# Kernel optimization log

Measured on AMD Instinct MI355X. Metric: run time of the kernel, lower is better.

Reference implementation:

```python
import jax, jax.numpy as jnp
import numpy as np

N, IN_F, HID, HEADS, OUT = 50000, 128, 32, 4, 40
E = 800000
LN_EPS = 1e-5


def setup_inputs() -> dict:
    key = jax.random.key(0)
    ks = jax.random.split(key, 16)
    d1 = HEADS * HID  # 128
    s_in = 1.0 / np.sqrt(IN_F)
    s_d1 = 1.0 / np.sqrt(d1)
    return {
        "x": jax.random.normal(ks[0], (N, IN_F), jnp.float32),
        "edge_index": jax.random.randint(ks[1], (2, E), 0, N, jnp.int64),
        # layer 1 (GATv2, heads=4, concat=True)
        "Wl1": jax.random.normal(ks[2], (IN_F, d1), jnp.float32) * s_in,
        "bl1": jnp.zeros((d1,), jnp.float32),
        "Wr1": jax.random.normal(ks[3], (IN_F, d1), jnp.float32) * s_in,
        "br1": jnp.zeros((d1,), jnp.float32),
        "att1": jax.random.normal(ks[4], (HEADS, HID), jnp.float32) * s_d1,
        "b1": jnp.zeros((d1,), jnp.float32),
        # LayerNorm over hidden_channels*heads
        "g1": jnp.ones((d1,), jnp.float32),
        "be1": jnp.zeros((d1,), jnp.float32),
        # layer 2 (GATv2, heads=1, concat=False)
        "Wl2": jax.random.normal(ks[5], (d1, OUT), jnp.float32) * s_d1,
        "bl2": jnp.zeros((OUT,), jnp.float32),
        "Wr2": jax.random.normal(ks[6], (d1, OUT), jnp.float32) * s_d1,
        "br2": jnp.zeros((OUT,), jnp.float32),
        "att2": jax.random.normal(ks[7], (1, OUT), jnp.float32) / np.sqrt(OUT),
        "b2": jnp.zeros((OUT,), jnp.float32),
    }


def gatv2(x, src, tgt, Wl, bl, Wr, br, att, bias, heads, C, concat):
    n = x.shape[0]
    xl = (x @ Wl + bl).reshape(n, heads, C)  # source transform
    xr = (x @ Wr + br).reshape(n, heads, C)  # target transform
    h = xl[src] + xr[tgt]                    # [E,H,C]
    e = jnp.sum(jax.nn.leaky_relu(h, 0.2) * att, axis=-1)  # [E,H]
    # segment softmax over edges sharing the same target node
    m = jax.ops.segment_max(e, tgt, num_segments=n)        # [N,H]
    m = jnp.where(jnp.isfinite(m), m, 0.0)
    p = jnp.exp(e - m[tgt])
    s = jax.ops.segment_sum(p, tgt, num_segments=n)
    alpha = p / (s[tgt] + 1e-16)                           # [E,H]
    out = jax.ops.segment_sum(alpha[..., None] * xl[src], tgt, num_segments=n)  # [N,H,C]
    out = out.reshape(n, heads * C) if concat else out.mean(axis=1)
    return out + bias


def layer_norm(x, g, b):
    mu = x.mean(-1, keepdims=True)
    var = x.var(-1, keepdims=True)
    return (x - mu) * jax.lax.rsqrt(var + LN_EPS) * g + b


def reference(x, edge_index, Wl1, bl1, Wr1, br1, att1, b1, g1, be1,
              Wl2, bl2, Wr2, br2, att2, b2):
    src, tgt = edge_index[0], edge_index[1]
    h = gatv2(x, src, tgt, Wl1, bl1, Wr1, br1, att1, b1, HEADS, HID, True)
    h = jax.nn.elu(layer_norm(h, g1, be1))
    # dropout is identity in eval mode
    return gatv2(h, src, tgt, Wl2, bl2, Wr2, br2, att2, b2, 1, OUT, False)
```

## Files before the change

kernel.cpp:

```cpp
#include <hip/hip_runtime.h>
#include <hip/hip_bf16.h>
#include <math.h>

#define NN 50000
#define EE 800000
#define NB_SCAN 49

typedef __attribute__((ext_vector_type(8))) short bf16x8;
typedef __attribute__((ext_vector_type(4))) float f32x4;
typedef __attribute__((ext_vector_type(2))) float f32x2;
typedef __attribute__((ext_vector_type(8))) unsigned short ushortx8;

#define OFF_XBF  ((size_t)0)
#define SZ_XBF   ((size_t)NN * 128 * 2)
#define OFF_XL1B (OFF_XBF + SZ_XBF)
#define SZ_XL1B  ((size_t)NN * 128 * 2)
#define OFF_XR1  (OFF_XL1B + SZ_XL1B)
#define SZ_XR1   ((size_t)NN * 128 * 4)
#define OFF_H1B  (OFF_XR1 + SZ_XR1)
#define SZ_H1B   ((size_t)NN * 128 * 2)
#define OFF_XL2B (OFF_H1B + SZ_H1B)
#define SZ_XL2B  ((size_t)NN * 40 * 2)
#define OFF_XR2  (OFF_XL2B + SZ_XL2B)
#define SZ_XR2   ((size_t)NN * 40 * 4)
#define OFF_BP1  (OFF_XR2 + SZ_XR2)
#define SZ_BP1   ((size_t)32768 * 2)
#define OFF_BP2  (OFF_BP1 + SZ_BP1)
#define SZ_BP2   ((size_t)10240 * 2)
#define OFF_BB1  (OFF_BP2 + SZ_BP2)
#define SZ_BB1   ((size_t)1024)
#define OFF_BB2  (OFF_BB1 + SZ_BB1)
#define SZ_BB2   ((size_t)512)
#define OFF_DEG  (OFF_BB2 + SZ_BB2)
#define SZ_DEG   ((size_t)NN * 4)
#define OFF_OFFS (OFF_DEG + SZ_DEG)
#define SZ_OFFS  ((size_t)200192)
#define OFF_CUR  (OFF_OFFS + SZ_OFFS)
#define SZ_CUR   ((size_t)NN * 4)
#define OFF_CSR  (OFF_CUR + SZ_CUR)
#define SZ_CSR   ((size_t)EE * 4)
#define OFF_BSUM (OFF_CSR + SZ_CSR)
#define SZ_BSUM  ((size_t)256)

__device__ __forceinline__ unsigned short f2bf(float f) {
    union { float f; unsigned u; } v;
    v.f = f;
    unsigned r = v.u + 0x7fffu + ((v.u >> 16) & 1u);
    return (unsigned short)(r >> 16);
}
__device__ __forceinline__ f32x2 bf2f2(unsigned u) {
    union { unsigned u; float f; } lo, hi;
    lo.u = u << 16;
    hi.u = u & 0xffff0000u;
    f32x2 r;
    r.x = lo.f;
    r.y = hi.f;
    return r;
}

__device__ __forceinline__ f32x2 pk_add(f32x2 a, f32x2 b) {
    f32x2 d;
    asm("v_pk_add_f32 %0, %1, %2" : "=v"(d) : "v"(a), "v"(b));
    return d;
}
__device__ __forceinline__ f32x2 pk_mul(f32x2 a, f32x2 b) {
    f32x2 d;
    asm("v_pk_mul_f32 %0, %1, %2" : "=v"(d) : "v"(a), "v"(b));
    return d;
}
__device__ __forceinline__ f32x2 pk_fma(f32x2 a, f32x2 b, f32x2 c) {
    f32x2 d;
    asm("v_pk_fma_f32 %0, %1, %2, %3" : "=v"(d) : "v"(a), "v"(b), "v"(c));
    return d;
}
__device__ __forceinline__ f32x2 pk_abs2(f32x2 a) {
    f32x2 r;
    r.x = __builtin_fabsf(a.x);
    r.y = __builtin_fabsf(a.y);
    return r;
}

__global__ void prep_kernel(
    const float* __restrict__ x, unsigned short* __restrict__ XBF,
    const float* __restrict__ Wl1, const float* __restrict__ bl1,
    const float* __restrict__ Wr1, const float* __restrict__ br1,
    const float* __restrict__ Wl2, const float* __restrict__ bl2,
    const float* __restrict__ Wr2, const float* __restrict__ br2,
    unsigned short* __restrict__ BP1, float* __restrict__ BB1,
    unsigned short* __restrict__ BP2, float* __restrict__ BB2,
    int* __restrict__ DEG) {
    int i = blockIdx.x * blockDim.x + threadIdx.x;
    if (i < NN * 128 / 8) {
        const float4* p = (const float4*)x + (size_t)i * 2;
        float4 v0 = p[0], v1 = p[1];
        ushortx8 o;
        o[0] = f2bf(v0.x); o[1] = f2bf(v0.y); o[2] = f2bf(v0.z); o[3] = f2bf(v0.w);
        o[4] = f2bf(v1.x); o[5] = f2bf(v1.y); o[6] = f2bf(v1.z); o[7] = f2bf(v1.w);
        *((ushortx8*)XBF + i) = o;
    }
    if (i < NN) DEG[i] = 0;
    if (i < 32768) {
        int j = i & 7, l = (i >> 3) & 63, nt = (i >> 9) & 15, kt = i >> 13;
        int k = kt * 32 + ((l >> 4) << 3) + j;
        int n = nt * 16 + (l & 15);
        float v = (n < 128) ? Wl1[k * 128 + n] : Wr1[k * 128 + (n - 128)];
        BP1[i] = f2bf(v);
    }
    if (i < 10240) {
        int j = i & 7, l = (i >> 3) & 63;
        int rest = i >> 9;
        int nt = rest % 5, kt = rest / 5;
        int k = kt * 32 + ((l >> 4) << 3) + j;
        int n = nt * 16 + (l & 15);
        float v = (n < 40) ? Wl2[k * 40 + n] : Wr2[k * 40 + (n - 40)];
        BP2[i] = f2bf(v);
    }
    if (i < 256) BB1[i] = (i < 128) ? bl1[i] : br1[i - 128];
    if (i < 80) BB2[i] = (i < 40) ? bl2[i] : br2[i - 40];
}

__global__ void hist_kernel(const int* __restrict__ tgts, int* __restrict__ deg, int e_) {
    int e = blockIdx.x * blockDim.x + threadIdx.x;
    if (e < e_) atomicAdd(&deg[tgts[e]], 1);
}

__global__ __launch_bounds__(1024) void scan_bsum_kernel(
    const int* __restrict__ deg, int* __restrict__ bsum, int n) {
    __shared__ int ws[16];
    int lane = threadIdx.x & 63, w = threadIdx.x >> 6;
    int i = blockIdx.x * 1024 + threadIdx.x;
    int v = (i < n) ? deg[i] : 0;
#pragma unroll
    for (int d = 32; d >= 1; d >>= 1) v += __shfl_xor(v, d, 64);
    if (lane == 0) ws[w] = v;
    __syncthreads();
    if (threadIdx.x < 16) {
        int xv = ws[threadIdx.x];
#pragma unroll
        for (int d = 8; d >= 1; d >>= 1) xv += __shfl_xor(xv, d, 16);
        if (threadIdx.x == 0) bsum[blockIdx.x] = xv;
    }
}

__global__ void scan_boff_kernel(int* __restrict__ bsum, int nb) {
    int tid = threadIdx.x;
    int v = (tid < nb) ? bsum[tid] : 0;
    int incl = v;
#pragma unroll
    for (int d = 1; d < 64; d <<= 1) {
        int t = __shfl_up(incl, d, 64);
        if (tid >= d) incl += t;
    }
    if (tid < nb) bsum[tid] = incl - v;
}

__global__ __launch_bounds__(1024) void scan_final_kernel(
    const int* __restrict__ deg, const int* __restrict__ bsum,
    int* __restrict__ off, int* __restrict__ cur, int n) {
    __shared__ int wsum[16];
    int lane = threadIdx.x & 63, w = threadIdx.x >> 6;
    int carry = bsum[blockIdx.x];
    int i = blockIdx.x * 1024 + threadIdx.x;
    int v = (i < n) ? deg[i] : 0;
    int incl = v;
#pragma unroll
    for (int d = 1; d < 64; d <<= 1) {
        int t = __shfl_up(incl, d, 64);
        if (lane >= d) incl += t;
    }
    if (lane == 63) wsum[w] = incl;
    __syncthreads();
    if (threadIdx.x < 16) {
        int xv = wsum[threadIdx.x];
#pragma unroll
        for (int d = 1; d < 16; d <<= 1) {
            int t = __shfl_up(xv, d, 16);
            if ((int)threadIdx.x >= d) xv += t;
        }
        wsum[threadIdx.x] = xv;
    }
    __syncthreads();
    int add = (w > 0) ? wsum[w - 1] : 0;
    if (i < n) {
        int tot = carry + incl + add;
        off[i + 1] = tot;
        cur[i] = tot - v;
    }
    if (i == 0) off[0] = 0;
}

__global__ void scatter_kernel(const int* __restrict__ srcs, const int* __restrict__ tgts,
                               int* __restrict__ cur, int* __restrict__ csr, int e_) {
    int e = blockIdx.x * blockDim.x + threadIdx.x;
    if (e < e_) {
        int t = tgts[e];
        int pos = atomicAdd(&cur[t], 1);
        csr[pos] = srcs[e];
    }
}

__global__ __launch_bounds__(256) void gemm_mfma_kernel(
    const unsigned short* __restrict__ Abf, const unsigned short* __restrict__ BP,
    const float* __restrict__ bias, unsigned short* __restrict__ Cbf,
    float* __restrict__ Cf, int M, int NT, int NSPLIT) {
    int wave = (blockIdx.x * blockDim.x + threadIdx.x) >> 6;
    int lane = threadIdx.x & 63;
    int r0 = wave * 16;
    if (r0 >= M) return;
    int koff = (lane >> 4) << 3;
    const unsigned short* ap = &Abf[(size_t)(r0 + (lane & 15)) * 128 + koff];
    bf16x8 a0 = *(const bf16x8*)(ap);
    bf16x8 a1 = *(const bf16x8*)(ap + 32);
    bf16x8 a2 = *(const bf16x8*)(ap + 64);
    bf16x8 a3 = *(const bf16x8*)(ap + 96);
    int NR = (NT << 4) - NSPLIT;
    int col = lane & 15;
    int rb = r0 + ((lane >> 4) << 2);
    size_t ktStride = (size_t)NT * 512;
    for (int nt = 0; nt < NT; ++nt) {
        const unsigned short* bp = &BP[((size_t)nt * 64 + lane) * 8];
        f32x4 acc = {0.f, 0.f, 0.f, 0.f};
        acc = __builtin_amdgcn_mfma_f32_16x16x32_bf16(a0, *(const bf16x8*)(bp), acc, 0, 0, 0);
        acc = __builtin_amdgcn_mfma_f32_16x16x32_bf16(a1, *(const bf16x8*)(bp + ktStride), acc, 0, 0, 0);
        acc = __builtin_amdgcn_mfma_f32_16x16x32_bf16(a2, *(const bf16x8*)(bp + 2 * ktStride), acc, 0, 0, 0);
        acc = __builtin_amdgcn_mfma_f32_16x16x32_bf16(a3, *(const bf16x8*)(bp + 3 * ktStride), acc, 0, 0, 0);
        int c = (nt << 4) + col;
        float bb = bias[c];
        if (c < NSPLIT) {
#pragma unroll
            for (int j = 0; j < 4; ++j) Cbf[(size_t)(rb + j) * NSPLIT + c] = f2bf(acc[j] + bb);
        } else {
#pragma unroll
            for (int j = 0; j < 4; ++j) Cf[(size_t)(rb + j) * NR + (c - NSPLIT)] = acc[j] + bb;
        }
    }
}

__global__ __launch_bounds__(256) void gat_edge1_kernel(
    const unsigned short* __restrict__ XL1B, const float* __restrict__ XR1,
    const int* __restrict__ off, const int* __restrict__ csr,
    const float* __restrict__ att, const float* __restrict__ b1,
    const float* __restrict__ g1, const float* __restrict__ be1,
    unsigned short* __restrict__ H1B) {
    int wid = threadIdx.x >> 6;
    int lane = threadIdx.x & 63;
    int node = blockIdx.x * 4 + wid;
    if (node >= NN) return;
    int grp = lane >> 4;
    int sub = lane & 15;
    int cbase = sub << 3;
    const float* xrrow = &XR1[(size_t)node * 128];
    float4 xrA = *(const float4*)&xrrow[cbase];
    float4 xrB = *(const float4*)&xrrow[cbase + 4];
    float4 atA = *(const float4*)&att[cbase];
    float4 atB = *(const float4*)&att[cbase + 4];
    f32x2 xr01 = {xrA.x, xrA.y}, xr23 = {xrA.z, xrA.w};
    f32x2 xr45 = {xrB.x, xrB.y}, xr67 = {xrB.z, xrB.w};
    f32x2 a06_01 = {0.6f * atA.x, 0.6f * atA.y}, a06_23 = {0.6f * atA.z, 0.6f * atA.w};
    f32x2 a06_45 = {0.6f * atB.x, 0.6f * atB.y}, a06_67 = {0.6f * atB.z, 0.6f * atB.w};
    f32x2 a04_01 = {0.4f * atA.x, 0.4f * atA.y}, a04_23 = {0.4f * atA.z, 0.4f * atA.w};
    f32x2 a04_45 = {0.4f * atB.x, 0.4f * atB.y}, a04_67 = {0.4f * atB.z, 0.4f * atB.w};
    f32x2 acc01 = {0.f, 0.f}, acc23 = {0.f, 0.f}, acc45 = {0.f, 0.f}, acc67 = {0.f, 0.f};
    float s = 0.f;
    int jb = off[node], je = off[node + 1];
    int nb = (je - jb + 3) >> 2;
#pragma unroll 2
    for (int k = 0; k < nb; ++k) {
        int eidx = jb + (k << 2) + grp;
        int src = csr[min(eidx, je - 1)];
        uint4 q = *(const uint4*)&XL1B[(size_t)src * 128 + cbase];
        f32x2 xl01 = bf2f2(q.x), xl23 = bf2f2(q.y), xl45 = bf2f2(q.z), xl67 = bf2f2(q.w);
        f32x2 h01 = pk_add(xl01, xr01);
        f32x2 h23 = pk_add(xl23, xr23);
        f32x2 h45 = pk_add(xl45, xr45);
        f32x2 h67 = pk_add(xl67, xr67);
        f32x2 t2 = pk_mul(h01, a06_01);
        t2 = pk_fma(pk_abs2(h01), a04_01, t2);
        t2 = pk_fma(h23, a06_23, t2);
        t2 = pk_fma(pk_abs2(h23), a04_23, t2);
        t2 = pk_fma(h45, a06_45, t2);
        t2 = pk_fma(pk_abs2(h45), a04_45, t2);
        t2 = pk_fma(h67, a06_67, t2);
        t2 = pk_fma(pk_abs2(h67), a04_67, t2);
        float t = t2.x + t2.y;
        t += __shfl_xor(t, 1, 64);
        t += __shfl_xor(t, 2, 64);
        t = (eidx < je) ? t : -1e30f;
        float p = __expf(t);
        f32x2 pp;
        pp.x = p;
        pp.y = p;
        acc01 = pk_fma(pp, xl01, acc01);
        acc23 = pk_fma(pp, xl23, acc23);
        acc45 = pk_fma(pp, xl45, acc45);
        acc67 = pk_fma(pp, xl67, acc67);
        s += p;
    }
    float a0 = acc01.x, a1 = acc01.y, a2 = acc23.x, a3 = acc23.y;
    float a4 = acc45.x, a5 = acc45.y, a6 = acc67.x, a7 = acc67.y;
#pragma unroll
    for (int d = 16; d <= 32; d <<= 1) {
        s += __shfl_xor(s, d, 64);
        a0 += __shfl_xor(a0, d, 64);
        a1 += __shfl_xor(a1, d, 64);
        a2 += __shfl_xor(a2, d, 64);
        a3 += __shfl_xor(a3, d, 64);
        a4 += __shfl_xor(a4, d, 64);
        a5 += __shfl_xor(a5, d, 64);
        a6 += __shfl_xor(a6, d, 64);
        a7 += __shfl_xor(a7, d, 64);
    }
    float inv = 1.f / (s + 1e-16f);
    float4 bA = *(const float4*)&b1[cbase];
    float4 bB = *(const float4*)&b1[cbase + 4];
    float o[8];
    o[0] = a0 * inv + bA.x;
    o[1] = a1 * inv + bA.y;
    o[2] = a2 * inv + bA.z;
    o[3] = a3 * inv + bA.w;
    o[4] = a4 * inv + bB.x;
    o[5] = a5 * inv + bB.y;
    o[6] = a6 * inv + bB.z;
    o[7] = a7 * inv + bB.w;
    float sum = 0.f, sq = 0.f;
#pragma unroll
    for (int j = 0; j < 8; ++j) {
        sum += o[j];
        sq = fmaf(o[j], o[j], sq);
    }
#pragma unroll
    for (int d = 1; d <= 8; d <<= 1) {
        sum += __shfl_xor(sum, d, 64);
        sq += __shfl_xor(sq, d, 64);
    }
    float mu = sum * (1.f / 128.f);
    float var = sq * (1.f / 128.f) - mu * mu;
    float rs = rsqrtf(var + 1e-5f);
    if (grp == 0) {
        float4 gA = *(const float4*)&g1[cbase];
        float4 gB = *(const float4*)&g1[cbase + 4];
        float4 eA = *(const float4*)&be1[cbase];
        float4 eB = *(const float4*)&be1[cbase + 4];
        float y[8];
        y[0] = (o[0] - mu) * rs * gA.x + eA.x;
        y[1] = (o[1] - mu) * rs * gA.y + eA.y;
        y[2] = (o[2] - mu) * rs * gA.z + eA.z;
        y[3] = (o[3] - mu) * rs * gA.w + eA.w;
        y[4] = (o[4] - mu) * rs * gB.x + eB.x;
        y[5] = (o[5] - mu) * rs * gB.y + eB.y;
        y[6] = (o[6] - mu) * rs * gB.z + eB.z;
        y[7] = (o[7] - mu) * rs * gB.w + eB.w;
        ushortx8 hw;
#pragma unroll
        for (int j = 0; j < 8; ++j) {
            float yy = y[j] > 0.f ? y[j] : expm1f(y[j]);
            hw[j] = f2bf(yy);
        }
        *(ushortx8*)&H1B[(size_t)node * 128 + cbase] = hw;
    }
}

__global__ __launch_bounds__(256) void gat_edge2_kernel(
    const unsigned short* __restrict__ XL2B, const float* __restrict__ XR2,
    const int* __restrict__ off, const int* __restrict__ csr,
    const float* __restrict__ att2, const float* __restrict__ b2,
    float* __restrict__ Y) {
    int wid = threadIdx.x >> 6;
    int lane = threadIdx.x & 63;
    int node = blockIdx.x * 4 + wid;
    if (node >= NN) return;
    int grp = lane >> 4;
    int sub = lane & 15;
    bool chact = sub < 10;
    int cbase = sub << 2;
    int cld = chact ? cbase : 0;
    float4 xr = make_float4(0.f, 0.f, 0.f, 0.f);
    float4 at = make_float4(0.f, 0.f, 0.f, 0.f);
    if (chact) {
        xr = *(const float4*)&XR2[(size_t)node * 40 + cbase];
        at = *(const float4*)&att2[cbase];
    }
    f32x2 xr01 = {xr.x, xr.y}, xr23 = {xr.z, xr.w};
    f32x2 a06_01 = {0.6f * at.x, 0.6f * at.y}, a06_23 = {0.6f * at.z, 0.6f * at.w};
    f32x2 a04_01 = {0.4f * at.x, 0.4f * at.y}, a04_23 = {0.4f * at.z, 0.4f * at.w};
    f32x2 acc01 = {0.f, 0.f}, acc23 = {0.f, 0.f};
    float s = 0.f;
    int jb = off[node], je = off[node + 1];
    int nb = (je - jb + 3) >> 2;
#pragma unroll 2
    for (int k = 0; k < nb; ++k) {
        int eidx = jb + (k << 2) + grp;
        int src = csr[min(eidx, je - 1)];
        uint2 q = *(const uint2*)&XL2B[(size_t)src * 40 + cld];
        f32x2 xl01 = bf2f2(q.x), xl23 = bf2f2(q.y);
        f32x2 h01 = pk_add(xl01, xr01);
        f32x2 h23 = pk_add(xl23, xr23);
        f32x2 t2 = pk_mul(h01, a06_01);
        t2 = pk_fma(pk_abs2(h01), a04_01, t2);
        t2 = pk_fma(h23, a06_23, t2);
        t2 = pk_fma(pk_abs2(h23), a04_23, t2);
        float t = t2.x + t2.y;
        t += __shfl_xor(t, 1, 64);
        t += __shfl_xor(t, 2, 64);
        t += __shfl_xor(t, 4, 64);
        t += __shfl_xor(t, 8, 64);
        t = (eidx < je) ? t : -1e30f;
        float p = __expf(t);
        f32x2 pp;
        pp.x = p;
        pp.y = p;
        acc01 = pk_fma(pp, xl01, acc01);
        acc23 = pk_fma(pp, xl23, acc23);
        s += p;
    }
    float a0 = acc01.x, a1 = acc01.y, a2 = acc23.x, a3 = acc23.y;
#pragma unroll
    for (int d = 16; d <= 32; d <<= 1) {
        s += __shfl_xor(s, d, 64);
        a0 += __shfl_xor(a0, d, 64);
        a1 += __shfl_xor(a1, d, 64);
        a2 += __shfl_xor(a2, d, 64);
        a3 += __shfl_xor(a3, d, 64);
    }
    if (grp == 0 && chact) {
        float inv = 1.f / (s + 1e-16f);
        float4 bb = *(const float4*)&b2[cbase];
        float4 y;
        y.x = a0 * inv + bb.x;
        y.y = a1 * inv + bb.y;
        y.z = a2 * inv + bb.z;
        y.w = a3 * inv + bb.w;
        *(float4*)&Y[(size_t)node * 40 + cbase] = y;
    }
}

extern "C" void kernel_launch(void* const* d_in, const int* in_sizes, int n_in,
                              void* d_out, int out_size, void* d_ws, size_t ws_size,
                              hipStream_t stream) {
    const float* x = (const float*)d_in[0];
    const int* ei = (const int*)d_in[1];
    const float* Wl1 = (const float*)d_in[2];
    const float* bl1 = (const float*)d_in[3];
    const float* Wr1 = (const float*)d_in[4];
    const float* br1 = (const float*)d_in[5];
    const float* att1 = (const float*)d_in[6];
    const float* b1 = (const float*)d_in[7];
    const float* g1 = (const float*)d_in[8];
    const float* be1 = (const float*)d_in[9];
    const float* Wl2 = (const float*)d_in[10];
    const float* bl2 = (const float*)d_in[11];
    const float* Wr2 = (const float*)d_in[12];
    const float* br2 = (const float*)d_in[13];
    const float* att2 = (const float*)d_in[14];
    const float* b2 = (const float*)d_in[15];

    const int* srcs = ei;
    const int* tgts = ei + EE;

    char* ws = (char*)d_ws;
    unsigned short* XBF = (unsigned short*)(ws + OFF_XBF);
    unsigned short* XL1B = (unsigned short*)(ws + OFF_XL1B);
    float* XR1 = (float*)(ws + OFF_XR1);
    unsigned short* H1B = (unsigned short*)(ws + OFF_H1B);
    unsigned short* XL2B = (unsigned short*)(ws + OFF_XL2B);
    float* XR2 = (float*)(ws + OFF_XR2);
    unsigned short* BP1 = (unsigned short*)(ws + OFF_BP1);
    unsigned short* BP2 = (unsigned short*)(ws + OFF_BP2);
    float* BB1 = (float*)(ws + OFF_BB1);
    float* BB2 = (float*)(ws + OFF_BB2);
    int* DEG = (int*)(ws + OFF_DEG);
    int* OFFS = (int*)(ws + OFF_OFFS);
    int* CUR = (int*)(ws + OFF_CUR);
    int* CSR = (int*)(ws + OFF_CSR);
    int* BSUM = (int*)(ws + OFF_BSUM);

    float* Y = (float*)d_out;

    prep_kernel<<<(NN * 128 / 8 + 255) / 256, 256, 0, stream>>>(
        x, XBF, Wl1, bl1, Wr1, br1, Wl2, bl2, Wr2, br2, BP1, BB1, BP2, BB2, DEG);

    hist_kernel<<<(EE + 255) / 256, 256, 0, stream>>>(tgts, DEG, EE);
    scan_bsum_kernel<<<NB_SCAN, 1024, 0, stream>>>(DEG, BSUM, NN);
    scan_boff_kernel<<<1, 64, 0, stream>>>(BSUM, NB_SCAN);
    scan_final_kernel<<<NB_SCAN, 1024, 0, stream>>>(DEG, BSUM, OFFS, CUR, NN);
    scatter_kernel<<<(EE + 255) / 256, 256, 0, stream>>>(srcs, tgts, CUR, CSR, EE);

    gemm_mfma_kernel<<<(3125 + 3) / 4, 256, 0, stream>>>(XBF, BP1, BB1, XL1B, XR1, NN, 16, 128);

    gat_edge1_kernel<<<(NN + 3) / 4, 256, 0, stream>>>(XL1B, XR1, OFFS, CSR, att1, b1, g1, be1, H1B);

    gemm_mfma_kernel<<<(3125 + 3) / 4, 256, 0, stream>>>(H1B, BP2, BB2, XL2B, XR2, NN, 5, 40);

    gat_edge2_kernel<<<(NN + 3) / 4, 256, 0, stream>>>(XL2B, XR2, OFFS, CSR, att2, b2, Y);
}
```

Before: 226.3 us.

## Batch neighbor index loads, use DPP reductions, fold scan offset kernel

```diff
diff --git a/kernel.cpp b/kernel.cpp
--- a/kernel.cpp
+++ b/kernel.cpp
@@ -80,6 +80,9 @@
     return r;
 }
 
+#define DPP_ADD(t, ctrl) \
+    ((t) + __int_as_float(__builtin_amdgcn_mov_dpp(__float_as_int(t), (ctrl), 0xF, 0xF, true)))
+
 __global__ void prep_kernel(
     const float* __restrict__ x, unsigned short* __restrict__ XBF,
     const float* __restrict__ Wl1, const float* __restrict__ bl1,
@@ -142,24 +145,18 @@
     }
 }
 
-__global__ void scan_boff_kernel(int* __restrict__ bsum, int nb) {
-    int tid = threadIdx.x;
-    int v = (tid < nb) ? bsum[tid] : 0;
-    int incl = v;
-#pragma unroll
-    for (int d = 1; d < 64; d <<= 1) {
-        int t = __shfl_up(incl, d, 64);
-        if (tid >= d) incl += t;
-    }
-    if (tid < nb) bsum[tid] = incl - v;
-}
-
 __global__ __launch_bounds__(1024) void scan_final_kernel(
     const int* __restrict__ deg, const int* __restrict__ bsum,
     int* __restrict__ off, int* __restrict__ cur, int n) {
     __shared__ int wsum[16];
+    __shared__ int carrySh;
     int lane = threadIdx.x & 63, w = threadIdx.x >> 6;
-    int carry = bsum[blockIdx.x];
+    if (threadIdx.x < 64) {
+        int v = ((int)threadIdx.x < (int)blockIdx.x) ? bsum[threadIdx.x] : 0;
+#pragma unroll
+        for (int d = 32; d >= 1; d >>= 1) v += __shfl_xor(v, d, 64);
+        if (threadIdx.x == 0) carrySh = v;
+    }
     int i = blockIdx.x * 1024 + threadIdx.x;
     int v = (i < n) ? deg[i] : 0;
     int incl = v;
@@ -181,6 +178,7 @@
     }
     __syncthreads();
     int add = (w > 0) ? wsum[w - 1] : 0;
+    int carry = carrySh;
     if (i < n) {
         int tot = carry + incl + add;
         off[i + 1] = tot;
@@ -256,36 +254,32 @@
     float4 atB = *(const float4*)&att[cbase + 4];
     f32x2 xr01 = {xrA.x, xrA.y}, xr23 = {xrA.z, xrA.w};
     f32x2 xr45 = {xrB.x, xrB.y}, xr67 = {xrB.z, xrB.w};
-    f32x2 a06_01 = {0.6f * atA.x, 0.6f * atA.y}, a06_23 = {0.6f * atA.z, 0.6f * atA.w};
-    f32x2 a06_45 = {0.6f * atB.x, 0.6f * atB.y}, a06_67 = {0.6f * atB.z, 0.6f * atB.w};
-    f32x2 a04_01 = {0.4f * atA.x, 0.4f * atA.y}, a04_23 = {0.4f * atA.z, 0.4f * atA.w};
-    f32x2 a04_45 = {0.4f * atB.x, 0.4f * atB.y}, a04_67 = {0.4f * atB.z, 0.4f * atB.w};
+    f32x2 at01 = {atA.x, atA.y}, at23 = {atA.z, atA.w};
+    f32x2 at45 = {atB.x, atB.y}, at67 = {atB.z, atB.w};
+    f32x2 c06 = {0.6f, 0.6f}, c04 = {0.4f, 0.4f};
     f32x2 acc01 = {0.f, 0.f}, acc23 = {0.f, 0.f}, acc45 = {0.f, 0.f}, acc67 = {0.f, 0.f};
     float s = 0.f;
     int jb = off[node], je = off[node + 1];
-    int nb = (je - jb + 3) >> 2;
-#pragma unroll 2
-    for (int k = 0; k < nb; ++k) {
-        int eidx = jb + (k << 2) + grp;
-        int src = csr[min(eidx, je - 1)];
-        uint4 q = *(const uint4*)&XL1B[(size_t)src * 128 + cbase];
+    int deg = je - jb;
+
+    auto process = [&](uint4 q, int eo) {
         f32x2 xl01 = bf2f2(q.x), xl23 = bf2f2(q.y), xl45 = bf2f2(q.z), xl67 = bf2f2(q.w);
         f32x2 h01 = pk_add(xl01, xr01);
         f32x2 h23 = pk_add(xl23, xr23);
         f32x2 h45 = pk_add(xl45, xr45);
         f32x2 h67 = pk_add(xl67, xr67);
-        f32x2 t2 = pk_mul(h01, a06_01);
-        t2 = pk_fma(pk_abs2(h01), a04_01, t2);
-        t2 = pk_fma(h23, a06_23, t2);
-        t2 = pk_fma(pk_abs2(h23), a04_23, t2);
-        t2 = pk_fma(h45, a06_45, t2);
-        t2 = pk_fma(pk_abs2(h45), a04_45, t2);
-        t2 = pk_fma(h67, a06_67, t2);
-        t2 = pk_fma(pk_abs2(h67), a04_67, t2);
+        f32x2 u01 = pk_fma(pk_abs2(h01), c04, pk_mul(h01, c06));
+        f32x2 u23 = pk_fma(pk_abs2(h23), c04, pk_mul(h23, c06));
+        f32x2 u45 = pk_fma(pk_abs2(h45), c04, pk_mul(h45, c06));
+        f32x2 u67 = pk_fma(pk_abs2(h67), c04, pk_mul(h67, c06));
+        f32x2 t2 = pk_mul(u01, at01);
+        t2 = pk_fma(u23, at23, t2);
+        t2 = pk_fma(u45, at45, t2);
+        t2 = pk_fma(u67, at67, t2);
         float t = t2.x + t2.y;
-        t += __shfl_xor(t, 1, 64);
-        t += __shfl_xor(t, 2, 64);
-        t = (eidx < je) ? t : -1e30f;
+        t = DPP_ADD(t, 0xB1);
+        t = DPP_ADD(t, 0x4E);
+        t = (eo < deg) ? t : -1e30f;
         float p = __expf(t);
         f32x2 pp;
         pp.x = p;
@@ -295,7 +289,24 @@
         acc45 = pk_fma(pp, xl45, acc45);
         acc67 = pk_fma(pp, xl67, acc67);
         s += p;
-    }
+    };
+
+    for (int ch = 0; ch < deg; ch += 16) {
+        int sidx = csr[min(jb + ch + sub, je - 1)];
+        int s0 = __shfl(sidx, grp, 16);
+        int s1 = __shfl(sidx, 4 + grp, 16);
+        int s2 = __shfl(sidx, 8 + grp, 16);
+        int s3 = __shfl(sidx, 12 + grp, 16);
+        uint4 q0 = *(const uint4*)&XL1B[(size_t)s0 * 128 + cbase];
+        uint4 q1 = *(const uint4*)&XL1B[(size_t)s1 * 128 + cbase];
+        uint4 q2 = *(const uint4*)&XL1B[(size_t)s2 * 128 + cbase];
+        uint4 q3 = *(const uint4*)&XL1B[(size_t)s3 * 128 + cbase];
+        process(q0, ch + grp);
+        process(q1, ch + 4 + grp);
+        process(q2, ch + 8 + grp);
+        process(q3, ch + 12 + grp);
+    }
+
     float a0 = acc01.x, a1 = acc01.y, a2 = acc23.x, a3 = acc23.y;
     float a4 = acc45.x, a5 = acc45.y, a6 = acc67.x, a7 = acc67.y;
 #pragma unroll
@@ -381,30 +392,27 @@
         at = *(const float4*)&att2[cbase];
     }
     f32x2 xr01 = {xr.x, xr.y}, xr23 = {xr.z, xr.w};
-    f32x2 a06_01 = {0.6f * at.x, 0.6f * at.y}, a06_23 = {0.6f * at.z, 0.6f * at.w};
-    f32x2 a04_01 = {0.4f * at.x, 0.4f * at.y}, a04_23 = {0.4f * at.z, 0.4f * at.w};
+    f32x2 at01 = {at.x, at.y}, at23 = {at.z, at.w};
+    f32x2 c06 = {0.6f, 0.6f}, c04 = {0.4f, 0.4f};
     f32x2 acc01 = {0.f, 0.f}, acc23 = {0.f, 0.f};
     float s = 0.f;
     int jb = off[node], je = off[node + 1];
-    int nb = (je - jb + 3) >> 2;
-#pragma unroll 2
-    for (int k = 0; k < nb; ++k) {
-        int eidx = jb + (k << 2) + grp;
-        int src = csr[min(eidx, je - 1)];
-        uint2 q = *(const uint2*)&XL2B[(size_t)src * 40 + cld];
+    int deg = je - jb;
+
+    auto process = [&](uint2 q, int eo) {
         f32x2 xl01 = bf2f2(q.x), xl23 = bf2f2(q.y);
         f32x2 h01 = pk_add(xl01, xr01);
         f32x2 h23 = pk_add(xl23, xr23);
-        f32x2 t2 = pk_mul(h01, a06_01);
-        t2 = pk_fma(pk_abs2(h01), a04_01, t2);
-        t2 = pk_fma(h23, a06_23, t2);
-        t2 = pk_fma(pk_abs2(h23), a04_23, t2);
+        f32x2 u01 = pk_fma(pk_abs2(h01), c04, pk_mul(h01, c06));
+        f32x2 u23 = pk_fma(pk_abs2(h23), c04, pk_mul(h23, c06));
+        f32x2 t2 = pk_mul(u01, at01);
+        t2 = pk_fma(u23, at23, t2);
         float t = t2.x + t2.y;
-        t += __shfl_xor(t, 1, 64);
-        t += __shfl_xor(t, 2, 64);
-        t += __shfl_xor(t, 4, 64);
-        t += __shfl_xor(t, 8, 64);
-        t = (eidx < je) ? t : -1e30f;
+        t = DPP_ADD(t, 0xB1);
+        t = DPP_ADD(t, 0x4E);
+        t = DPP_ADD(t, 0x124);
+        t = DPP_ADD(t, 0x128);
+        t = (eo < deg) ? t : -1e30f;
         float p = __expf(t);
         f32x2 pp;
         pp.x = p;
@@ -412,7 +420,24 @@
         acc01 = pk_fma(pp, xl01, acc01);
         acc23 = pk_fma(pp, xl23, acc23);
         s += p;
-    }
+    };
+
+    for (int ch = 0; ch < deg; ch += 16) {
+        int sidx = csr[min(jb + ch + sub, je - 1)];
+        int s0 = __shfl(sidx, grp, 16);
+        int s1 = __shfl(sidx, 4 + grp, 16);
+        int s2 = __shfl(sidx, 8 + grp, 16);
+        int s3 = __shfl(sidx, 12 + grp, 16);
+        uint2 q0 = *(const uint2*)&XL2B[(size_t)s0 * 40 + cld];
+        uint2 q1 = *(const uint2*)&XL2B[(size_t)s1 * 40 + cld];
+        uint2 q2 = *(const uint2*)&XL2B[(size_t)s2 * 40 + cld];
+        uint2 q3 = *(const uint2*)&XL2B[(size_t)s3 * 40 + cld];
+        process(q0, ch + grp);
+        process(q1, ch + 4 + grp);
+        process(q2, ch + 8 + grp);
+        process(q3, ch + 12 + grp);
+    }
+
     float a0 = acc01.x, a1 = acc01.y, a2 = acc23.x, a3 = acc23.y;
 #pragma unroll
     for (int d = 16; d <= 32; d <<= 1) {
@@ -481,7 +506,6 @@
 
     hist_kernel<<<(EE + 255) / 256, 256, 0, stream>>>(tgts, DEG, EE);
     scan_bsum_kernel<<<NB_SCAN, 1024, 0, stream>>>(DEG, BSUM, NN);
-    scan_boff_kernel<<<1, 64, 0, stream>>>(BSUM, NB_SCAN);
     scan_final_kernel<<<NB_SCAN, 1024, 0, stream>>>(DEG, BSUM, OFFS, CUR, NN);
     scatter_kernel<<<(EE + 255) / 256, 256, 0, stream>>>(srcs, tgts, CUR, CSR, EE);
 
```

Result: faster. 202.1 us (-10.7%).
